# Kernel optimization log

Measured on AMD Instinct MI355X. Metric: run time of the kernel, lower is better.

The kernel has to match this reference:

```python
import jax, jax.numpy as jnp
import numpy as np
from jax import lax

VOCAB = 32000
EMBED = 1024
HIDDEN = 1024
ML = 64          # config.MAX_LENGTH
L = 50           # input sentence length
HH = HIDDEN // 2 # per-direction encoder hidden


def _lstm_cell(x, h, c, Wih, Whh, bih, bhh):
    # torch LSTM gate order: i, f, g, o
    g = x @ Wih.T + h @ Whh.T + bih + bhh
    i, f, gg, o = jnp.split(g, 4)
    i = jax.nn.sigmoid(i)
    f = jax.nn.sigmoid(f)
    gg = jnp.tanh(gg)
    o = jax.nn.sigmoid(o)
    c = f * c + i * gg
    return o * jnp.tanh(c), c


def setup_inputs() -> dict:
    key = jax.random.key(0)
    ks = jax.random.split(key, 24)
    def n(k, shape, s=0.05):
        return jax.random.normal(k, shape, jnp.float32) * s
    return {
        "x_tokens": jax.random.randint(ks[0], (L,), 0, VOCAB, jnp.int32),
        "allowed_mask": jnp.ones((VOCAB + ML,), jnp.float32),
        "embedding": n(ks[1], (VOCAB, EMBED)),
        # encoder bi-LSTM (two cells, each hidden//2)
        "Wih_f": n(ks[2], (4 * HH, EMBED)), "Whh_f": n(ks[3], (4 * HH, HH)),
        "bih_f": n(ks[4], (4 * HH,)), "bhh_f": n(ks[5], (4 * HH,)),
        "Wih_b": n(ks[6], (4 * HH, EMBED)), "Whh_b": n(ks[7], (4 * HH, HH)),
        "bih_b": n(ks[8], (4 * HH,)), "bhh_b": n(ks[9], (4 * HH,)),
        # decoder LSTM: input = embed + 2*hidden
        "Wih_d": n(ks[10], (4 * HIDDEN, EMBED + 2 * HIDDEN)),
        "Whh_d": n(ks[11], (4 * HIDDEN, HIDDEN)),
        "bih_d": n(ks[12], (4 * HIDDEN,)), "bhh_d": n(ks[13], (4 * HIDDEN,)),
        # attention: Linear(2*hidden -> MAX_LENGTH)
        "attn_W": n(ks[14], (ML, 2 * HIDDEN)), "attn_b": n(ks[15], (ML,)),
        # generate layer: Linear(hidden -> vocab)
        "gen_W": n(ks[16], (VOCAB, HIDDEN)), "gen_b": n(ks[17], (VOCAB,)),
        # copy layer: Linear(hidden -> hidden)
        "copy_W": n(ks[18], (HIDDEN, HIDDEN)), "copy_b": n(ks[19], (HIDDEN,)),
    }


def _forward(allowed_mask, embedding, Wih_f, Whh_f, bih_f, bhh_f,
             Wih_b, Whh_b, bih_b, bhh_b, Wih_d, Whh_d, bih_d, bhh_d,
             attn_W, attn_b, gen_W, gen_b, copy_W, copy_b, x_tokens):
    xemb = embedding[x_tokens]  # (L, EMBED)

    # --- encoder: two LSTM cells both stepped forward-in-time (as in the
    # original, where the bidirectional LSTM is called one token at a time) ---
    def enc_step(carry, xe):
        hf, cf, hb, cb = carry
        hf, cf = _lstm_cell(xe, hf, cf, Wih_f, Whh_f, bih_f, bhh_f)
        hb, cb = _lstm_cell(xe, hb, cb, Wih_b, Whh_b, bih_b, bhh_b)
        return (hf, cf, hb, cb), jnp.concatenate([hf, hb])

    z = jnp.zeros((HH,), xemb.dtype)
    (hf, cf, hb, cb), enc = lax.scan(enc_step, (z, z, z, z), xemb)
    enc_outs = jnp.zeros((ML, HIDDEN), xemb.dtype).at[:L].set(enc)  # padded buffer
    h0 = jnp.concatenate([hf, hb])  # (HIDDEN,) decoder init
    c0 = jnp.concatenate([cf, cb])

    copy_enc = jnp.tanh(enc_outs @ copy_W.T + copy_b)  # (ML, HIDDEN), loop-invariant
    pos = jnp.arange(ML)
    sent_pad = jnp.full((ML,), -1, jnp.int32).at[:L].set(x_tokens)
    sos_emb = embedding[0]

    def dec_step(carry, t):
        h, c, prev_probs, prev_word, dec_in = carry
        first = t == 0
        # attentive read
        a = jnp.concatenate([dec_in, h])  # (2*HIDDEN,)
        attw = jax.nn.softmax(a @ attn_W.T + attn_b)
        attentive = attw @ enc_outs  # (HIDDEN,)
        # selective (copy) read from previous step's copy probs
        pc = prev_probs[VOCAB:]
        m = ((pos >= 1) & (pos < L - 1) & (sent_pad != prev_word)).astype(pc.dtype)
        pc = pc * m
        s = pc.sum()
        pc = jnp.where(s > 0, pc / jnp.where(s > 0, s, 1.0), pc)
        selective = pc @ enc_outs
        zero = jnp.zeros_like(attentive)
        attentive = jnp.where(first, zero, attentive)
        selective = jnp.where(first, zero, selective)
        # decoder LSTM step
        h, c = _lstm_cell(jnp.concatenate([dec_in, selective, attentive]),
                          h, c, Wih_d, Whh_d, bih_d, bhh_d)
        gen = h @ gen_W.T + gen_b        # (VOCAB,)
        copy = copy_enc @ h              # (ML,)
        probs = jax.nn.softmax(jnp.concatenate([gen, copy]))
        dist = probs * allowed_mask
        # deterministic action (argmax in place of Categorical.sample)
        aidx = jnp.argmax(dist)
        is_voc = aidx < VOCAB
        src = sent_pad[jnp.clip(aidx - VOCAB, 0, L - 1)]
        action = jnp.where(is_voc, aidx, src).astype(jnp.int32)
        prob = dist[aidx] + jnp.where(
            is_voc, jnp.zeros((), dist.dtype), dist[jnp.clip(action, 0, VOCAB - 1)])
        new = (h, c, lax.stop_gradient(probs), action, embedding[action])
        return new, (h, prob, action)

    carry0 = (h0, c0, jnp.zeros((VOCAB + ML,), h0.dtype),
              jnp.array(-1, jnp.int32), sos_emb)
    _, (hs, probs, actions) = lax.scan(dec_step, carry0, jnp.arange(ML))
    states = jnp.concatenate([h0[None], hs])  # (ML+1, HIDDEN)
    return states, probs, actions


def reference(x_tokens, allowed_mask, embedding, Wih_f, Whh_f, bih_f, bhh_f,
              Wih_b, Whh_b, bih_b, bhh_b, Wih_d, Whh_d, bih_d, bhh_d,
              attn_W, attn_b, gen_W, gen_b, copy_W, copy_b):
    return _forward(allowed_mask, embedding, Wih_f, Whh_f, bih_f, bhh_f,
                    Wih_b, Whh_b, bih_b, bhh_b, Wih_d, Whh_d, bih_d, bhh_d,
                    attn_W, attn_b, gen_W, gen_b, copy_W, copy_b, x_tokens)
```

## Files before the change

kernel.cpp:

```cpp
#include <hip/hip_runtime.h>
#include <math.h>

#define L 50
#define ML 64
#define VOCAB 32000
#define EMBED 1024
#define HID 1024
#define HH 512
#define TOT (VOCAB+ML)
#define NPART 501

#define WS_ENC_GATES 0
#define WS_C_ENC     8192
#define WS_ENC_OUTS  10240
#define WS_COPY_ENC  75776
#define WS_H_DEC     141312
#define WS_C_DEC     143360
#define WS_X_DEC     145408
#define WS_DGATES    148480
#define WS_LOGITS    152576
#define WS_PARTS     184640
#define WS_ATTW      186688
#define WS_PC        186752

__device__ __forceinline__ float wred_sum(float v){
  #pragma unroll
  for(int o=32;o;o>>=1) v += __shfl_xor(v,o,64);
  return v;
}
__device__ __forceinline__ float wred_max(float v){
  #pragma unroll
  for(int o=32;o;o>>=1) v = fmaxf(v,__shfl_xor(v,o,64));
  return v;
}
__device__ __forceinline__ float sigm(float x){ return 1.0f/(1.0f+__expf(-x)); }
__device__ __forceinline__ float d4(float4 a, float4 b){ return a.x*b.x + a.y*b.y + a.z*b.z + a.w*b.w; }

__global__ __launch_bounds__(256) void k_enc_step(
  const int* __restrict__ xt, const float* __restrict__ emb,
  const float* __restrict__ Wih_f, const float* __restrict__ Whh_f,
  const float* __restrict__ bih_f, const float* __restrict__ bhh_f,
  const float* __restrict__ Wih_b, const float* __restrict__ Whh_b,
  const float* __restrict__ bih_b, const float* __restrict__ bhh_b,
  float* __restrict__ ws, int t)
{
  __shared__ __align__(16) float h_lds[1024];
  __shared__ __align__(16) float xe[1024];
  const int tid = threadIdx.x;
  float* gates   = ws + WS_ENC_GATES;
  float* c_enc   = ws + WS_C_ENC;
  float* enc_outs= ws + WS_ENC_OUTS;
  {
    const int tok = xt[t];
    const float* er = emb + (size_t)tok*EMBED;
    for(int j=tid;j<1024;j+=256) xe[j]=er[j];
  }
  if(t>0){
    const float* gp = gates + ((t-1)&1)*4096;
    const float* cp = c_enc + (t&1)*1024;
    float* cw = c_enc + ((t-1)&1)*1024;
    for(int u=tid;u<1024;u+=256){
      int base = (u<512)?0:2048;
      int uu   = (u<512)?u:(u-512);
      float ig=gp[base+uu], fg=gp[base+512+uu], gg=gp[base+1024+uu], og=gp[base+1536+uu];
      float cprev = (t==1)?0.0f:cp[u];
      float c = sigm(fg)*cprev + sigm(ig)*tanhf(gg);
      float h = sigm(og)*tanhf(c);
      h_lds[u]=h;
      if(blockIdx.x==0){
        cw[u]=c;
        enc_outs[(size_t)(t-1)*1024+u]=h;
      }
    }
  }
  __syncthreads();
  float* gw = gates + (t&1)*4096;
  const int wave=tid>>6, lane=tid&63;
  for(int rr=0;rr<2;rr++){
    int r = blockIdx.x*8 + wave*2 + rr;
    bool isF = (r<2048);
    int rl = isF? r : r-2048;
    const float* Wih = isF? Wih_f : Wih_b;
    const float* Whh = isF? Whh_f : Whh_b;
    float bias = isF? (bih_f[rl]+bhh_f[rl]) : (bih_b[rl]+bhh_b[rl]);
    const float* wr = Wih + (size_t)rl*EMBED;
    float acc=0.0f;
    #pragma unroll
    for(int c4=0;c4<4;c4++){
      int m=c4*256+lane*4;
      acc += d4(*(const float4*)(wr+m), *(const float4*)(&xe[m]));
    }
    if(t>0){
      const float* hr = Whh + (size_t)rl*HH;
      const float* hs = &h_lds[isF?0:512];
      #pragma unroll
      for(int c4=0;c4<2;c4++){
        int m=c4*256+lane*4;
        acc += d4(*(const float4*)(hr+m), *(const float4*)(&hs[m]));
      }
    }
    acc = wred_sum(acc);
    if(lane==0) gw[r]=acc+bias;
  }
}

__global__ __launch_bounds__(256) void k_enc_final(float* __restrict__ ws, float* __restrict__ out)
{
  const int tid=threadIdx.x;
  float* gates = ws + WS_ENC_GATES;
  float* c_enc = ws + WS_C_ENC;
  float* enc_outs = ws + WS_ENC_OUTS;
  float* h_dec = ws + WS_H_DEC;
  float* c_dec = ws + WS_C_DEC;
  const float* gp = gates + ((L-1)&1)*4096;
  const float* cp = c_enc + ((L-2)&1)*1024;
  for(int u=tid;u<1024;u+=256){
    int base=(u<512)?0:2048;
    int uu=(u<512)?u:(u-512);
    float ig=gp[base+uu], fg=gp[base+512+uu], gg=gp[base+1024+uu], og=gp[base+1536+uu];
    float c = sigm(fg)*cp[u] + sigm(ig)*tanhf(gg);
    float h = sigm(og)*tanhf(c);
    enc_outs[(size_t)(L-1)*1024+u]=h;
    h_dec[1024+u]=h;
    c_dec[1024+u]=c;
    out[u]=h;
  }
  for(int j=tid;j<(ML-L)*1024;j+=256) enc_outs[(size_t)L*1024+j]=0.0f;
}

__global__ __launch_bounds__(256) void k_copy_enc(
  const float* __restrict__ copy_W, const float* __restrict__ copy_b, float* __restrict__ ws)
{
  float* enc_outs = ws+WS_ENC_OUTS;
  float* cenc = ws+WS_COPY_ENC;
  const int wave=threadIdx.x>>6, lane=threadIdx.x&63;
  int j = blockIdx.x*4 + wave;
  const float* wr = copy_W + (size_t)j*1024;
  float4 w0=*(const float4*)(wr+0*256+lane*4);
  float4 w1=*(const float4*)(wr+1*256+lane*4);
  float4 w2=*(const float4*)(wr+2*256+lane*4);
  float4 w3=*(const float4*)(wr+3*256+lane*4);
  float bj = copy_b[j];
  for(int k=0;k<ML;k++){
    const float* er = enc_outs + (size_t)k*1024;
    float acc = d4(w0,*(const float4*)(er+0*256+lane*4))
              + d4(w1,*(const float4*)(er+1*256+lane*4))
              + d4(w2,*(const float4*)(er+2*256+lane*4))
              + d4(w3,*(const float4*)(er+3*256+lane*4));
    acc = wred_sum(acc);
    if(lane==0) cenc[(size_t)k*1024+j]=tanhf(acc+bj);
  }
}

__global__ __launch_bounds__(256) void k_dec_init(const float* __restrict__ emb, float* __restrict__ ws)
{
  float* x_dec=ws+WS_X_DEC;
  for(int j=threadIdx.x;j<1024;j+=256){
    x_dec[j]=emb[j];
    x_dec[1024+j]=0.0f;
    x_dec[2048+j]=0.0f;
  }
}

__global__ __launch_bounds__(256) void k_attn(
  const int* __restrict__ xt, const float* __restrict__ amask,
  const float* __restrict__ emb,
  const float* __restrict__ attn_W, const float* __restrict__ attn_b,
  float* __restrict__ ws, float* __restrict__ out, int t, int fin_only)
{
  __shared__ __align__(16) float dec_in[1024];
  __shared__ __align__(16) float hprev[1024];
  __shared__ float r_lm[256], r_sm[256], r_ky[256];
  __shared__ int r_ix[256];
  __shared__ float s_lmax, s_Z;
  __shared__ int s_act;
  const int tid=threadIdx.x;
  float* h_dec=ws+WS_H_DEC; float* x_dec=ws+WS_X_DEC;
  float* logits=ws+WS_LOGITS; float* parts=ws+WS_PARTS;
  float* attw_raw=ws+WS_ATTW; float* pcw=ws+WS_PC;

  {
    float lm=-INFINITY, sm=0.0f, ky=-INFINITY; int ix=0x7fffffff;
    for(int i=tid;i<NPART;i+=256){
      const float4 p = *(const float4*)(parts+(size_t)i*4);
      float plm=p.x, psm=p.y, pky=p.z; int pix=__float_as_int(p.w);
      if(plm>lm){ sm = sm*__expf(lm-plm)+psm; lm=plm; }
      else sm += psm*__expf(plm-lm);
      if(pky>ky || (pky==ky && pix<ix)){ ky=pky; ix=pix; }
    }
    r_lm[tid]=lm; r_sm[tid]=sm; r_ky[tid]=ky; r_ix[tid]=ix;
    __syncthreads();
    for(int s=128;s;s>>=1){
      if(tid<s){
        float blm=r_lm[tid+s], bsm=r_sm[tid+s];
        float alm=r_lm[tid], a_sm=r_sm[tid];
        if(blm>alm){ r_sm[tid]=a_sm*__expf(alm-blm)+bsm; r_lm[tid]=blm; }
        else r_sm[tid]=a_sm+bsm*__expf(blm-alm);
        float bky=r_ky[tid+s]; int bix=r_ix[tid+s];
        if(bky>r_ky[tid] || (bky==r_ky[tid] && bix<r_ix[tid])){ r_ky[tid]=bky; r_ix[tid]=bix; }
      }
      __syncthreads();
    }
    if(tid==0){
      float lmax=r_lm[0]; float Z=r_sm[0];
      float bky=r_ky[0];
      int aidx = (bky==-INFINITY)?0:r_ix[0];
      bool isv = aidx<VOCAB;
      int kcl = aidx-VOCAB; kcl = kcl<0?0:(kcl>(L-1)?(L-1):kcl);
      int sp = xt[kcl];
      int action = isv? aidx : sp;
      if(blockIdx.x==0){
        float prob = amask[aidx]*__expf(logits[aidx]-lmax)/Z;
        if(!isv){
          int a2 = action<0?0:(action>(VOCAB-1)?(VOCAB-1):action);
          prob += amask[a2]*__expf(logits[a2]-lmax)/Z;
        }
        out[65*1024 + (t-1)] = prob;
        out[65*1024 + 64 + (t-1)] = (float)action;
      }
      s_lmax=lmax; s_Z=Z; s_act=action;
    }
  }
  __syncthreads();
  if(fin_only) return;

  const int action = s_act;
  if(blockIdx.x==0 && tid<64){
    int k=tid;
    float v=__expf(logits[VOCAB+k]-s_lmax)/s_Z;
    int sp=(k<L)? xt[k] : -1;
    float m=(k>=1 && k<(L-1) && sp!=action)?1.0f:0.0f;
    float pv=v*m;
    float s=wred_sum(pv);
    pcw[k]=(s>0.0f)? pv/s : pv;
  }
  {
    int row = action<0 ? action+VOCAB : action;
    const float* er = emb + (size_t)row*EMBED;
    const float* hp = h_dec + ((t-1)&1)*1024;
    for(int j=tid;j<1024;j+=256){
      float v=er[j];
      dec_in[j]=v; hprev[j]=hp[j];
      if(blockIdx.x==0) x_dec[j]=v;
    }
  }
  __syncthreads();
  if(tid<64){
    const int lane=tid;
    const float* wr = attn_W + (size_t)blockIdx.x*2048;
    float acc=0.0f;
    #pragma unroll
    for(int c4=0;c4<4;c4++){
      int m=c4*256+lane*4;
      acc += d4(*(const float4*)(wr+m),      *(const float4*)(&dec_in[m]));
      acc += d4(*(const float4*)(wr+1024+m), *(const float4*)(&hprev[m]));
    }
    acc=wred_sum(acc);
    if(lane==0) attw_raw[blockIdx.x]=acc+attn_b[blockIdx.x];
  }
}

__global__ __launch_bounds__(256) void k_prep(float* __restrict__ ws)
{
  __shared__ float attw_s[64], pc_s[64];
  const int tid=threadIdx.x;
  float* enc_outs=ws+WS_ENC_OUTS; float* x_dec=ws+WS_X_DEC;
  float* attw_raw=ws+WS_ATTW; float* pcw=ws+WS_PC;
  if(tid<64){
    float v=attw_raw[tid];
    float mx=wred_max(v);
    float e=__expf(v-mx);
    float s=wred_sum(e);
    attw_s[tid]=e/s;
    pc_s[tid]=pcw[tid];
  }
  __syncthreads();
  int j=blockIdx.x*256+tid;
  float aA=0.0f, aS=0.0f;
  for(int k=0;k<ML;k++){
    float e=enc_outs[(size_t)k*1024+j];
    aA += attw_s[k]*e;
    aS += pc_s[k]*e;
  }
  x_dec[1024+j]=aS;
  x_dec[2048+j]=aA;
}

__global__ __launch_bounds__(256) void k_dec_gates(
  const float* __restrict__ Wih_d, const float* __restrict__ Whh_d,
  const float* __restrict__ bih_d, const float* __restrict__ bhh_d,
  float* __restrict__ ws, int t)
{
  __shared__ __align__(16) float x_lds[4096];
  const int tid=threadIdx.x;
  float* x_dec=ws+WS_X_DEC; float* h_dec=ws+WS_H_DEC; float* dg=ws+WS_DGATES;
  for(int j=tid;j<3072;j+=256) x_lds[j]=x_dec[j];
  {
    const float* hp=h_dec+((t+1)&1)*1024;
    for(int j=tid;j<1024;j+=256) x_lds[3072+j]=hp[j];
  }
  __syncthreads();
  const int wave=tid>>6, lane=tid&63;
  for(int rr=0;rr<2;rr++){
    int r=blockIdx.x*8+wave*2+rr;
    const float* wr=Wih_d+(size_t)r*3072;
    float acc=0.0f;
    #pragma unroll
    for(int c4=0;c4<12;c4++){
      int m=c4*256+lane*4;
      acc += d4(*(const float4*)(wr+m), *(const float4*)(&x_lds[m]));
    }
    const float* hr=Whh_d+(size_t)r*1024;
    #pragma unroll
    for(int c4=0;c4<4;c4++){
      int m=c4*256+lane*4;
      acc += d4(*(const float4*)(hr+m), *(const float4*)(&x_lds[3072+m]));
    }
    acc=wred_sum(acc);
    if(lane==0) dg[r]=acc+bih_d[r]+bhh_d[r];
  }
}

__global__ __launch_bounds__(256) void k_dec_gen(
  const float* __restrict__ gen_W, const float* __restrict__ gen_b,
  const float* __restrict__ amask,
  float* __restrict__ ws, float* __restrict__ out, int t)
{
  __shared__ __align__(16) float h_lds[1024];
  __shared__ float w_lm[4], w_sm[4], w_ky[4];
  __shared__ int w_ix[4];
  const int tid=threadIdx.x;
  float* dg=ws+WS_DGATES;
  float* c_dec=ws+WS_C_DEC; float* h_dec=ws+WS_H_DEC;
  float* logits=ws+WS_LOGITS; float* parts=ws+WS_PARTS;
  float* cenc=ws+WS_COPY_ENC;
  {
    const float* cp=c_dec+((t+1)&1)*1024;
    float* cw=c_dec+(t&1)*1024;
    float* hw=h_dec+(t&1)*1024;
    for(int u=tid;u<1024;u+=256){
      float ig=dg[u], fg=dg[1024+u], gg=dg[2048+u], og=dg[3072+u];
      float c=sigm(fg)*cp[u]+sigm(ig)*tanhf(gg);
      float h=sigm(og)*tanhf(c);
      h_lds[u]=h;
      if(blockIdx.x==0){ cw[u]=c; hw[u]=h; out[(size_t)(t+1)*1024+u]=h; }
    }
  }
  __syncthreads();
  const int wave=tid>>6, lane=tid&63;
  const int b=blockIdx.x;
  const bool isGen=(b<500);
  const int rbase = isGen ? (b*64+wave*16) : (VOCAB+wave*16);
  float lv[16];
  #pragma unroll
  for(int rr=0;rr<16;rr++){
    const float* wr = isGen ? gen_W+(size_t)(rbase+rr)*1024
                            : cenc +(size_t)(rbase-VOCAB+rr)*1024;
    float acc=0.0f;
    #pragma unroll
    for(int c4=0;c4<4;c4++){
      int m=c4*256+lane*4;
      acc += d4(*(const float4*)(wr+m), *(const float4*)(&h_lds[m]));
    }
    acc=wred_sum(acc);
    lv[rr] = isGen ? acc+gen_b[rbase+rr] : acc;
  }
  if(lane==0){
    float lm=-INFINITY, ky=-INFINITY; int ix=0;
    #pragma unroll
    for(int rr=0;rr<16;rr++){
      int gi=rbase+rr;
      logits[gi]=lv[rr];
      lm=fmaxf(lm,lv[rr]);
      float mk=amask[gi];
      float kk = (mk>0.0f)? (lv[rr]+__logf(mk)) : -INFINITY;
      if(kk>ky){ ky=kk; ix=gi; }
    }
    float sm=0.0f;
    #pragma unroll
    for(int rr=0;rr<16;rr++) sm += __expf(lv[rr]-lm);
    w_lm[wave]=lm; w_sm[wave]=sm; w_ky[wave]=ky; w_ix[wave]=ix;
  }
  __syncthreads();
  if(tid==0){
    float lm=w_lm[0], sm=w_sm[0], ky=w_ky[0]; int ix=w_ix[0];
    for(int w=1;w<4;w++){
      float blm=w_lm[w], bsm=w_sm[w];
      if(blm>lm){ sm=sm*__expf(lm-blm)+bsm; lm=blm; }
      else sm += bsm*__expf(blm-lm);
      if(w_ky[w]>ky || (w_ky[w]==ky && w_ix[w]<ix)){ ky=w_ky[w]; ix=w_ix[w]; }
    }
    float4 p; p.x=lm; p.y=sm; p.z=ky; p.w=__int_as_float(ix);
    *(float4*)(parts+(size_t)blockIdx.x*4)=p;
  }
}

extern "C" void kernel_launch(void* const* d_in, const int* in_sizes, int n_in,
                              void* d_out, int out_size, void* d_ws, size_t ws_size,
                              hipStream_t stream)
{
  const int*   xt     = (const int*)d_in[0];
  const float* amask  = (const float*)d_in[1];
  const float* emb    = (const float*)d_in[2];
  const float* Wih_f  = (const float*)d_in[3];
  const float* Whh_f  = (const float*)d_in[4];
  const float* bih_f  = (const float*)d_in[5];
  const float* bhh_f  = (const float*)d_in[6];
  const float* Wih_b  = (const float*)d_in[7];
  const float* Whh_b  = (const float*)d_in[8];
  const float* bih_b  = (const float*)d_in[9];
  const float* bhh_b  = (const float*)d_in[10];
  const float* Wih_d  = (const float*)d_in[11];
  const float* Whh_d  = (const float*)d_in[12];
  const float* bih_d  = (const float*)d_in[13];
  const float* bhh_d  = (const float*)d_in[14];
  const float* attn_W = (const float*)d_in[15];
  const float* attn_b = (const float*)d_in[16];
  const float* gen_W  = (const float*)d_in[17];
  const float* gen_b  = (const float*)d_in[18];
  const float* copy_W = (const float*)d_in[19];
  const float* copy_b = (const float*)d_in[20];
  float* out=(float*)d_out;
  float* ws =(float*)d_ws;

  for(int t=0;t<L;t++)
    k_enc_step<<<512,256,0,stream>>>(xt,emb,Wih_f,Whh_f,bih_f,bhh_f,Wih_b,Whh_b,bih_b,bhh_b,ws,t);
  k_enc_final<<<1,256,0,stream>>>(ws,out);
  k_copy_enc<<<256,256,0,stream>>>(copy_W,copy_b,ws);

  k_dec_init<<<1,256,0,stream>>>(emb,ws);
  k_dec_gates<<<512,256,0,stream>>>(Wih_d,Whh_d,bih_d,bhh_d,ws,0);
  k_dec_gen  <<<501,256,0,stream>>>(gen_W,gen_b,amask,ws,out,0);
  for(int t=1;t<ML;t++){
    k_attn     <<<64,256,0,stream>>>(xt,amask,emb,attn_W,attn_b,ws,out,t,0);
    k_prep     <<<4,256,0,stream>>>(ws);
    k_dec_gates<<<512,256,0,stream>>>(Wih_d,Whh_d,bih_d,bhh_d,ws,t);
    k_dec_gen  <<<501,256,0,stream>>>(gen_W,gen_b,amask,ws,out,t);
  }
  k_attn<<<1,256,0,stream>>>(xt,amask,emb,attn_W,attn_b,ws,out,ML,1);
}
```

Measured before the change: 3.728 ms.

## Hoist encoder input projections, fuse encoder tail, copy layer and attention prep

Precomputes the encoder's input-to-gate projections for all 50 tokens in one kernel, so each recurrent step only does the small hidden-state matvec. It fuses the encoder finalisation, decoder init and copy-layer projection into one launch, and skips the copy matvec on zero-padded rows by writing tanh(bias). It also merges attention scoring and context preparation into one kernel per decoder step, with each block recomputing all 64 attention rows redundantly. This removes launches from the serial chain at the cost of redundant work and a larger workspace, with a fallback path when the workspace is too small.

```diff
diff --git a/kernel.cpp b/kernel.cpp
--- a/kernel.cpp
+++ b/kernel.cpp
@@ -20,8 +20,8 @@
 #define WS_DGATES    148480
 #define WS_LOGITS    152576
 #define WS_PARTS     184640
-#define WS_ATTW      186688
-#define WS_PC        186752
+#define WS_PREG      186880
+#define WS_PREG_END  (186880+50*4096)
 
 __device__ __forceinline__ float wred_sum(float v){
   #pragma unroll
@@ -35,6 +35,87 @@
 }
 __device__ __forceinline__ float sigm(float x){ return 1.0f/(1.0f+__expf(-x)); }
 __device__ __forceinline__ float d4(float4 a, float4 b){ return a.x*b.x + a.y*b.y + a.z*b.z + a.w*b.w; }
+
+__global__ __launch_bounds__(256) void k_enc_pre(
+  const int* __restrict__ xt, const float* __restrict__ emb,
+  const float* __restrict__ Wih_f, const float* __restrict__ bih_f, const float* __restrict__ bhh_f,
+  const float* __restrict__ Wih_b, const float* __restrict__ bih_b, const float* __restrict__ bhh_b,
+  float* __restrict__ ws)
+{
+  __shared__ __align__(16) float xe[1024];
+  const int tid=threadIdx.x, b=blockIdx.x, wave=tid>>6, lane=tid&63;
+  float* pg = ws + WS_PREG;
+  float4 wih[2][4]; float bias[2];
+  #pragma unroll
+  for(int rr=0;rr<2;rr++){
+    int r=b*8+wave*2+rr; bool isF=(r<2048); int rl=isF?r:(r-2048);
+    const float* wp=(isF?Wih_f:Wih_b)+(size_t)rl*EMBED;
+    #pragma unroll
+    for(int c4=0;c4<4;c4++) wih[rr][c4]=*(const float4*)(wp+c4*256+lane*4);
+    bias[rr]= isF?(bih_f[rl]+bhh_f[rl]):(bih_b[rl]+bhh_b[rl]);
+  }
+  for(int t=0;t<L;t++){
+    const float* er = emb + (size_t)xt[t]*EMBED;
+    for(int j=tid;j<1024;j+=256) xe[j]=er[j];
+    __syncthreads();
+    #pragma unroll
+    for(int rr=0;rr<2;rr++){
+      int r=b*8+wave*2+rr;
+      float acc=0.0f;
+      #pragma unroll
+      for(int c4=0;c4<4;c4++) acc += d4(wih[rr][c4], *(const float4*)(&xe[c4*256+lane*4]));
+      acc=wred_sum(acc);
+      if(lane==0) pg[(size_t)t*4096+r]=acc+bias[rr];
+    }
+    __syncthreads();
+  }
+}
+
+__global__ __launch_bounds__(256) void k_enc_rec(
+  const float* __restrict__ Whh_f, const float* __restrict__ Whh_b,
+  float* __restrict__ ws, int t)
+{
+  __shared__ __align__(16) float h_lds[1024];
+  const int tid=threadIdx.x, b=blockIdx.x, wave=tid>>6, lane=tid&63;
+  float* gates   = ws + WS_ENC_GATES;
+  float* c_enc   = ws + WS_C_ENC;
+  float* enc_outs= ws + WS_ENC_OUTS;
+  const float* pg = ws + WS_PREG + (size_t)t*4096;
+  if(t>0){
+    const float* gp = gates + ((t-1)&1)*4096;
+    const float* cp = c_enc + (t&1)*1024;
+    float* cw = c_enc + ((t-1)&1)*1024;
+    for(int u=tid;u<1024;u+=256){
+      int base=(u<512)?0:2048, uu=(u<512)?u:(u-512);
+      float ig=gp[base+uu], fg=gp[base+512+uu], gg=gp[base+1024+uu], og=gp[base+1536+uu];
+      float cprev=(t==1)?0.0f:cp[u];
+      float c=sigm(fg)*cprev+sigm(ig)*tanhf(gg);
+      float h=sigm(og)*tanhf(c);
+      h_lds[u]=h;
+      if(b==0){ cw[u]=c; enc_outs[(size_t)(t-1)*1024+u]=h; }
+    }
+  }
+  __syncthreads();
+  float* gw = gates + (t&1)*4096;
+  #pragma unroll
+  for(int rr=0;rr<2;rr++){
+    int r=b*8+wave*2+rr; bool isF=(r<2048); int rl=isF?r:(r-2048);
+    if(t==0){
+      if(lane==0) gw[r]=pg[r];
+    } else {
+      const float* hr=(isF?Whh_f:Whh_b)+(size_t)rl*HH;
+      const float* hs=&h_lds[isF?0:512];
+      float acc=0.0f;
+      #pragma unroll
+      for(int c2=0;c2<2;c2++){
+        int m=c2*256+lane*4;
+        acc += d4(*(const float4*)(hr+m), *(const float4*)(&hs[m]));
+      }
+      acc=wred_sum(acc);
+      if(lane==0) gw[r]=pg[r]+acc;
+    }
+  }
+}
 
 __global__ __launch_bounds__(256) void k_enc_step(
   const int* __restrict__ xt, const float* __restrict__ emb,
@@ -60,30 +141,25 @@
     const float* cp = c_enc + (t&1)*1024;
     float* cw = c_enc + ((t-1)&1)*1024;
     for(int u=tid;u<1024;u+=256){
-      int base = (u<512)?0:2048;
-      int uu   = (u<512)?u:(u-512);
+      int base=(u<512)?0:2048, uu=(u<512)?u:(u-512);
       float ig=gp[base+uu], fg=gp[base+512+uu], gg=gp[base+1024+uu], og=gp[base+1536+uu];
-      float cprev = (t==1)?0.0f:cp[u];
-      float c = sigm(fg)*cprev + sigm(ig)*tanhf(gg);
-      float h = sigm(og)*tanhf(c);
+      float cprev=(t==1)?0.0f:cp[u];
+      float c=sigm(fg)*cprev+sigm(ig)*tanhf(gg);
+      float h=sigm(og)*tanhf(c);
       h_lds[u]=h;
-      if(blockIdx.x==0){
-        cw[u]=c;
-        enc_outs[(size_t)(t-1)*1024+u]=h;
-      }
+      if(blockIdx.x==0){ cw[u]=c; enc_outs[(size_t)(t-1)*1024+u]=h; }
     }
   }
   __syncthreads();
   float* gw = gates + (t&1)*4096;
   const int wave=tid>>6, lane=tid&63;
   for(int rr=0;rr<2;rr++){
-    int r = blockIdx.x*8 + wave*2 + rr;
-    bool isF = (r<2048);
-    int rl = isF? r : r-2048;
-    const float* Wih = isF? Wih_f : Wih_b;
-    const float* Whh = isF? Whh_f : Whh_b;
-    float bias = isF? (bih_f[rl]+bhh_f[rl]) : (bih_b[rl]+bhh_b[rl]);
-    const float* wr = Wih + (size_t)rl*EMBED;
+    int r=blockIdx.x*8+wave*2+rr;
+    bool isF=(r<2048); int rl=isF?r:(r-2048);
+    const float* Wih=isF?Wih_f:Wih_b;
+    const float* Whh=isF?Whh_f:Whh_b;
+    float bias=isF?(bih_f[rl]+bhh_f[rl]):(bih_b[rl]+bhh_b[rl]);
+    const float* wr=Wih+(size_t)rl*EMBED;
     float acc=0.0f;
     #pragma unroll
     for(int c4=0;c4<4;c4++){
@@ -91,57 +167,65 @@
       acc += d4(*(const float4*)(wr+m), *(const float4*)(&xe[m]));
     }
     if(t>0){
-      const float* hr = Whh + (size_t)rl*HH;
-      const float* hs = &h_lds[isF?0:512];
+      const float* hr=Whh+(size_t)rl*HH;
+      const float* hs=&h_lds[isF?0:512];
       #pragma unroll
-      for(int c4=0;c4<2;c4++){
-        int m=c4*256+lane*4;
+      for(int c2=0;c2<2;c2++){
+        int m=c2*256+lane*4;
         acc += d4(*(const float4*)(hr+m), *(const float4*)(&hs[m]));
       }
     }
-    acc = wred_sum(acc);
+    acc=wred_sum(acc);
     if(lane==0) gw[r]=acc+bias;
   }
 }
 
-__global__ __launch_bounds__(256) void k_enc_final(float* __restrict__ ws, float* __restrict__ out)
-{
-  const int tid=threadIdx.x;
+__global__ __launch_bounds__(256) void k_copy_final(
+  const float* __restrict__ emb,
+  const float* __restrict__ copy_W, const float* __restrict__ copy_b,
+  float* __restrict__ ws, float* __restrict__ out)
+{
+  __shared__ __align__(16) float hf[1024];
+  const int tid=threadIdx.x, b=blockIdx.x, wave=tid>>6, lane=tid&63;
   float* gates = ws + WS_ENC_GATES;
   float* c_enc = ws + WS_C_ENC;
   float* enc_outs = ws + WS_ENC_OUTS;
+  float* cenc = ws + WS_COPY_ENC;
   float* h_dec = ws + WS_H_DEC;
   float* c_dec = ws + WS_C_DEC;
-  const float* gp = gates + ((L-1)&1)*4096;
-  const float* cp = c_enc + ((L-2)&1)*1024;
-  for(int u=tid;u<1024;u+=256){
-    int base=(u<512)?0:2048;
-    int uu=(u<512)?u:(u-512);
-    float ig=gp[base+uu], fg=gp[base+512+uu], gg=gp[base+1024+uu], og=gp[base+1536+uu];
-    float c = sigm(fg)*cp[u] + sigm(ig)*tanhf(gg);
-    float h = sigm(og)*tanhf(c);
-    enc_outs[(size_t)(L-1)*1024+u]=h;
-    h_dec[1024+u]=h;
-    c_dec[1024+u]=c;
-    out[u]=h;
-  }
-  for(int j=tid;j<(ML-L)*1024;j+=256) enc_outs[(size_t)L*1024+j]=0.0f;
-}
-
-__global__ __launch_bounds__(256) void k_copy_enc(
-  const float* __restrict__ copy_W, const float* __restrict__ copy_b, float* __restrict__ ws)
-{
-  float* enc_outs = ws+WS_ENC_OUTS;
-  float* cenc = ws+WS_COPY_ENC;
-  const int wave=threadIdx.x>>6, lane=threadIdx.x&63;
-  int j = blockIdx.x*4 + wave;
+  float* x_dec = ws + WS_X_DEC;
+  {
+    const float* gp = gates + ((L-1)&1)*4096;
+    const float* cp = c_enc + ((L-2)&1)*1024;
+    for(int u=tid;u<1024;u+=256){
+      int base=(u<512)?0:2048, uu=(u<512)?u:(u-512);
+      float ig=gp[base+uu], fg=gp[base+512+uu], gg=gp[base+1024+uu], og=gp[base+1536+uu];
+      float c=sigm(fg)*cp[u]+sigm(ig)*tanhf(gg);
+      float h=sigm(og)*tanhf(c);
+      hf[u]=h;
+      if(b==0){
+        enc_outs[(size_t)(L-1)*1024+u]=h;
+        h_dec[1024+u]=h;
+        c_dec[1024+u]=c;
+        out[u]=h;
+      }
+    }
+    if(b==1) for(int j=tid;j<(ML-L)*1024;j+=256) enc_outs[(size_t)L*1024+j]=0.0f;
+    if(b==2) for(int j=tid;j<1024;j+=256){
+      x_dec[j]=emb[j];
+      x_dec[1024+j]=0.0f;
+      x_dec[2048+j]=0.0f;
+    }
+  }
+  __syncthreads();
+  int j = b*4 + wave;
   const float* wr = copy_W + (size_t)j*1024;
   float4 w0=*(const float4*)(wr+0*256+lane*4);
   float4 w1=*(const float4*)(wr+1*256+lane*4);
   float4 w2=*(const float4*)(wr+2*256+lane*4);
   float4 w3=*(const float4*)(wr+3*256+lane*4);
   float bj = copy_b[j];
-  for(int k=0;k<ML;k++){
+  for(int k=0;k<L-1;k++){
     const float* er = enc_outs + (size_t)k*1024;
     float acc = d4(w0,*(const float4*)(er+0*256+lane*4))
               + d4(w1,*(const float4*)(er+1*256+lane*4))
@@ -150,19 +234,21 @@
     acc = wred_sum(acc);
     if(lane==0) cenc[(size_t)k*1024+j]=tanhf(acc+bj);
   }
-}
-
-__global__ __launch_bounds__(256) void k_dec_init(const float* __restrict__ emb, float* __restrict__ ws)
-{
-  float* x_dec=ws+WS_X_DEC;
-  for(int j=threadIdx.x;j<1024;j+=256){
-    x_dec[j]=emb[j];
-    x_dec[1024+j]=0.0f;
-    x_dec[2048+j]=0.0f;
-  }
-}
-
-__global__ __launch_bounds__(256) void k_attn(
+  {
+    float acc = d4(w0,*(const float4*)(&hf[0*256+lane*4]))
+              + d4(w1,*(const float4*)(&hf[1*256+lane*4]))
+              + d4(w2,*(const float4*)(&hf[2*256+lane*4]))
+              + d4(w3,*(const float4*)(&hf[3*256+lane*4]));
+    acc = wred_sum(acc);
+    if(lane==0) cenc[(size_t)(L-1)*1024+j]=tanhf(acc+bj);
+  }
+  if(lane==0){
+    float z=tanhf(0.0f+bj);
+    for(int k=L;k<ML;k++) cenc[(size_t)k*1024+j]=z;
+  }
+}
+
+__global__ __launch_bounds__(256) void k_attn_prep(
   const int* __restrict__ xt, const float* __restrict__ amask,
   const float* __restrict__ emb,
   const float* __restrict__ attn_W, const float* __restrict__ attn_b,
@@ -172,12 +258,13 @@
   __shared__ __align__(16) float hprev[1024];
   __shared__ float r_lm[256], r_sm[256], r_ky[256];
   __shared__ int r_ix[256];
+  __shared__ float attw_raw[64], attw_s[64], pc_s[64];
   __shared__ float s_lmax, s_Z;
   __shared__ int s_act;
-  const int tid=threadIdx.x;
+  const int tid=threadIdx.x, b=blockIdx.x, wave=tid>>6, lane=tid&63;
   float* h_dec=ws+WS_H_DEC; float* x_dec=ws+WS_X_DEC;
   float* logits=ws+WS_LOGITS; float* parts=ws+WS_PARTS;
-  float* attw_raw=ws+WS_ATTW; float* pcw=ws+WS_PC;
+  float* enc_outs=ws+WS_ENC_OUTS;
 
   {
     float lm=-INFINITY, sm=0.0f, ky=-INFINITY; int ix=0x7fffffff;
@@ -209,7 +296,7 @@
       int kcl = aidx-VOCAB; kcl = kcl<0?0:(kcl>(L-1)?(L-1):kcl);
       int sp = xt[kcl];
       int action = isv? aidx : sp;
-      if(blockIdx.x==0){
+      if(b==0){
         float prob = amask[aidx]*__expf(logits[aidx]-lmax)/Z;
         if(!isv){
           int a2 = action<0?0:(action>(VOCAB-1)?(VOCAB-1):action);
@@ -225,14 +312,14 @@
   if(fin_only) return;
 
   const int action = s_act;
-  if(blockIdx.x==0 && tid<64){
+  if(tid<64){
     int k=tid;
     float v=__expf(logits[VOCAB+k]-s_lmax)/s_Z;
     int sp=(k<L)? xt[k] : -1;
     float m=(k>=1 && k<(L-1) && sp!=action)?1.0f:0.0f;
     float pv=v*m;
     float s=wred_sum(pv);
-    pcw[k]=(s>0.0f)? pv/s : pv;
+    pc_s[k]=(s>0.0f)? pv/s : pv;
   }
   {
     int row = action<0 ? action+VOCAB : action;
@@ -241,13 +328,13 @@
     for(int j=tid;j<1024;j+=256){
       float v=er[j];
       dec_in[j]=v; hprev[j]=hp[j];
-      if(blockIdx.x==0) x_dec[j]=v;
-    }
-  }
-  __syncthreads();
-  if(tid<64){
-    const int lane=tid;
-    const float* wr = attn_W + (size_t)blockIdx.x*2048;
+      if(b==0) x_dec[j]=v;
+    }
+  }
+  __syncthreads();
+  for(int rr=0;rr<16;rr++){
+    int r=wave*16+rr;
+    const float* wr = attn_W + (size_t)r*2048;
     float acc=0.0f;
     #pragma unroll
     for(int c4=0;c4<4;c4++){
@@ -256,34 +343,28 @@
       acc += d4(*(const float4*)(wr+1024+m), *(const float4*)(&hprev[m]));
     }
     acc=wred_sum(acc);
-    if(lane==0) attw_raw[blockIdx.x]=acc+attn_b[blockIdx.x];
-  }
-}
-
-__global__ __launch_bounds__(256) void k_prep(float* __restrict__ ws)
-{
-  __shared__ float attw_s[64], pc_s[64];
-  const int tid=threadIdx.x;
-  float* enc_outs=ws+WS_ENC_OUTS; float* x_dec=ws+WS_X_DEC;
-  float* attw_raw=ws+WS_ATTW; float* pcw=ws+WS_PC;
+    if(lane==0) attw_raw[r]=acc+attn_b[r];
+  }
+  __syncthreads();
   if(tid<64){
     float v=attw_raw[tid];
     float mx=wred_max(v);
     float e=__expf(v-mx);
     float s=wred_sum(e);
     attw_s[tid]=e/s;
-    pc_s[tid]=pcw[tid];
-  }
-  __syncthreads();
-  int j=blockIdx.x*256+tid;
-  float aA=0.0f, aS=0.0f;
-  for(int k=0;k<ML;k++){
-    float e=enc_outs[(size_t)k*1024+j];
-    aA += attw_s[k]*e;
-    aS += pc_s[k]*e;
-  }
-  x_dec[1024+j]=aS;
-  x_dec[2048+j]=aA;
+  }
+  __syncthreads();
+  if(tid<16){
+    int j=b*16+tid;
+    float aA=0.0f, aS=0.0f;
+    for(int k=0;k<ML;k++){
+      float e=enc_outs[(size_t)k*1024+j];
+      aA += attw_s[k]*e;
+      aS += pc_s[k]*e;
+    }
+    x_dec[1024+j]=aS;
+    x_dec[2048+j]=aA;
+  }
 }
 
 __global__ __launch_bounds__(256) void k_dec_gates(
@@ -423,19 +504,23 @@
   float* out=(float*)d_out;
   float* ws =(float*)d_ws;
 
-  for(int t=0;t<L;t++)
-    k_enc_step<<<512,256,0,stream>>>(xt,emb,Wih_f,Whh_f,bih_f,bhh_f,Wih_b,Whh_b,bih_b,bhh_b,ws,t);
-  k_enc_final<<<1,256,0,stream>>>(ws,out);
-  k_copy_enc<<<256,256,0,stream>>>(copy_W,copy_b,ws);
-
-  k_dec_init<<<1,256,0,stream>>>(emb,ws);
+  const bool big = ws_size >= (size_t)WS_PREG_END*sizeof(float);
+  if(big){
+    k_enc_pre<<<512,256,0,stream>>>(xt,emb,Wih_f,bih_f,bhh_f,Wih_b,bih_b,bhh_b,ws);
+    for(int t=0;t<L;t++)
+      k_enc_rec<<<512,256,0,stream>>>(Whh_f,Whh_b,ws,t);
+  } else {
+    for(int t=0;t<L;t++)
+      k_enc_step<<<512,256,0,stream>>>(xt,emb,Wih_f,Whh_f,bih_f,bhh_f,Wih_b,Whh_b,bih_b,bhh_b,ws,t);
+  }
+  k_copy_final<<<256,256,0,stream>>>(emb,copy_W,copy_b,ws,out);
+
   k_dec_gates<<<512,256,0,stream>>>(Wih_d,Whh_d,bih_d,bhh_d,ws,0);
   k_dec_gen  <<<501,256,0,stream>>>(gen_W,gen_b,amask,ws,out,0);
   for(int t=1;t<ML;t++){
-    k_attn     <<<64,256,0,stream>>>(xt,amask,emb,attn_W,attn_b,ws,out,t,0);
-    k_prep     <<<4,256,0,stream>>>(ws);
+    k_attn_prep<<<64,256,0,stream>>>(xt,amask,emb,attn_W,attn_b,ws,out,t,0);
     k_dec_gates<<<512,256,0,stream>>>(Wih_d,Whh_d,bih_d,bhh_d,ws,t);
     k_dec_gen  <<<501,256,0,stream>>>(gen_W,gen_b,amask,ws,out,t);
   }
-  k_attn<<<1,256,0,stream>>>(xt,amask,emb,attn_W,attn_b,ws,out,ML,1);
-}
+  k_attn_prep<<<1,256,0,stream>>>(xt,amask,emb,attn_W,attn_b,ws,out,ML,1);
+}
```

Result: slower. 4.658 ms (+24.9%).
